# Kernel optimization log

Measured on AMD Instinct MI355X. Metric: run time of the kernel, lower is better.

## Reference

```python
import jax, jax.numpy as jnp
import numpy as np

VOCAB, E, H, L, B, T, S, V = 32000, 512, 1024, 2, 64, 64, 128, 1024
LSTM_IN = 2 * E  # input_feed=True -> cat(embed, prev_output)


def setup_inputs() -> dict:
    key = jax.random.key(0)
    ks = jax.random.split(key, 12)
    s = lambda *d: 1.0 / np.sqrt(d[-1])
    return {
        "tgt_batch": jax.random.randint(ks[0], (T, B), 0, VOCAB),
        "h_encoder": jax.random.normal(ks[1], (B, S, V), jnp.float32),
        "emb": jax.random.normal(ks[2], (VOCAB, E), jnp.float32) * 0.02,
        "output_init": jnp.zeros((B, E), jnp.float32),
        "hidden_init": jnp.zeros((L, B, H), jnp.float32),
        "W_ih": jax.random.uniform(ks[3], (L, 4 * H, LSTM_IN), jnp.float32, -s(H), s(H)),
        "W_hh": jax.random.uniform(ks[4], (L, 4 * H, H), jnp.float32, -s(H), s(H)),
        "b_ih": jax.random.uniform(ks[5], (L, 4 * H), jnp.float32, -s(H), s(H)),
        "b_hh": jax.random.uniform(ks[6], (L, 4 * H), jnp.float32, -s(H), s(H)),
        "W1": jax.random.uniform(ks[7], (V, H), jnp.float32, -s(H), s(H)),   # query_size->values_size
        "b1": jnp.zeros((V,), jnp.float32),
        "W2": jax.random.uniform(ks[8], (E, H + V), jnp.float32, -s(H + V), s(H + V)),
        "b2": jnp.zeros((E,), jnp.float32),
    }


def reference(tgt_batch, h_encoder, emb, output_init, hidden_init,
              W_ih, W_hh, b_ih, b_hh, W1, b1, W2, b2):
    x_seq = emb[tgt_batch]  # [T, B, E]

    def lstm_cell(x, h, c):  # x:[B,2E], h/c:[L,B,H]
        hs, cs, inp = [], [], x
        for l in range(L):
            gates = inp @ W_ih[l].T + b_ih[l] + h[l] @ W_hh[l].T + b_hh[l]
            i, f, g, o = jnp.split(gates, 4, axis=-1)  # torch gate order i,f,g,o
            c_new = jax.nn.sigmoid(f) * c[l] + jax.nn.sigmoid(i) * jnp.tanh(g)
            h_new = jax.nn.sigmoid(o) * jnp.tanh(c_new)
            hs.append(h_new); cs.append(c_new); inp = h_new
        return jnp.stack(hs), jnp.stack(cs), inp

    def global_attn(query):  # query:[B,H]
        q = query @ W1.T + b1                              # [B,V]
        scores = jnp.einsum('bv,bsv->bs', q, h_encoder)    # [B,S]
        a = jax.nn.softmax(scores, axis=-1)
        attended = jnp.einsum('bs,bsv->bv', a, h_encoder)  # [B,V]
        return jnp.tanh(jnp.concatenate([attended, query], axis=-1) @ W2.T + b2)

    def step(carry, x):
        h, c, out = carry
        inp = jnp.concatenate([x, out], axis=-1)  # input feed
        h, c, top = lstm_cell(inp, h, c)
        o = global_attn(top)  # dropout is identity in eval mode
        return (h, c, o), o

    c0 = jnp.zeros_like(hidden_init)
    _, outs = jax.lax.scan(step, (hidden_init, c0, output_init), x_seq)
    return jnp.transpose(outs, (1, 0, 2))  # [B, T, E]
```

## Files before the change

### kernel.cpp

```cpp
#include <hip/hip_runtime.h>

typedef _Float16 f16;
typedef f16 f16x8 __attribute__((ext_vector_type(8)));
typedef f16 f16x2 __attribute__((ext_vector_type(2)));
typedef float f32x4 __attribute__((ext_vector_type(4)));
typedef unsigned long long u64;

#define MFMA16(a, b, c) __builtin_amdgcn_mfma_f32_16x16x32_f16(a, b, c, 0, 0, 0)
#define ROT 16

__device__ inline float fsig(float x) { return 1.f / (1.f + __expf(-x)); }
__device__ inline float ftanh(float x) {
    x = fminf(15.f, fmaxf(-15.f, x));
    float e = __expf(2.f * x);
    return (e - 1.f) / (e + 1.f);
}

__device__ __forceinline__ void bstore8(void* p, u64 v) {
    __hip_atomic_store((u64*)p, v, __ATOMIC_RELAXED, __HIP_MEMORY_SCOPE_AGENT);
}
__device__ __forceinline__ void bstore4(float* p, float v) {
    __hip_atomic_store(p, v, __ATOMIC_RELAXED, __HIP_MEMORY_SCOPE_AGENT);
}
__device__ __forceinline__ float bload_f32(const float* p) {
    return __hip_atomic_load((float*)p, __ATOMIC_RELAXED, __HIP_MEMORY_SCOPE_AGENT);
}
__device__ __forceinline__ void fstore_u32(unsigned* p, unsigned v) {
    __hip_atomic_store(p, v, __ATOMIC_RELAXED, __HIP_MEMORY_SCOPE_AGENT);
}
__device__ __forceinline__ unsigned fload_u32(unsigned* p) {
    return __hip_atomic_load(p, __ATOMIC_RELAXED, __HIP_MEMORY_SCOPE_AGENT);
}

__global__ __launch_bounds__(256) void k_convert(
    const float* __restrict__ Wih, const float* __restrict__ Whh,
    const float* __restrict__ W1, const float* __restrict__ W2,
    const float* __restrict__ bih, const float* __restrict__ bhh,
    const int* __restrict__ tgt, const float* __restrict__ emb,
    const float* __restrict__ henc,
    f16* __restrict__ wcat, f16* __restrict__ w1c, f16* __restrict__ w2a,
    f16* __restrict__ w2b, float* __restrict__ bsum, f16* __restrict__ Xall,
    f16* __restrict__ h16)
{
    const long NW = 16777216, NT = 1048576, NA = 524288, NB = 524288,
               NS = 8192, NX = 2097152, NH = 8388608;
    const long TOT = NW + NT + NA + NB + NS + NX + NH;
    for (long i = (long)blockIdx.x * 256 + threadIdx.x; i < TOT;
         i += (long)gridDim.x * 256) {
        if (i < NW) {
            long l = i >> 23;
            long r = i & 8388607;
            int j = (int)(r >> 11), k = (int)(r & 2047);
            float val = (k < 1024) ? Wih[(l * 4096 + j) * 1024 + k]
                                   : Whh[(l * 4096 + j) * 1024 + (k - 1024)];
            wcat[i] = (f16)val;
        } else if (i < NW + NT) {
            long r = i - NW;
            int h = (int)(r >> 10), v = (int)(r & 1023);
            w1c[r] = (f16)W1[(long)v * 1024 + h];
        } else if (i < NW + NT + NA) {
            long r = i - NW - NT;
            int e = (int)(r >> 10), v = (int)(r & 1023);
            w2a[r] = (f16)W2[(long)e * 2048 + v];
        } else if (i < NW + NT + NA + NB) {
            long r = i - NW - NT - NA;
            int e = (int)(r >> 10), k = (int)(r & 1023);
            w2b[r] = (f16)W2[(long)e * 2048 + 1024 + k];
        } else if (i < NW + NT + NA + NB + NS) {
            long r = i - NW - NT - NA - NB;
            bsum[r] = bih[r] + bhh[r];
        } else if (i < NW + NT + NA + NB + NS + NX) {
            long r = i - NW - NT - NA - NB - NS;
            int t = (int)(r >> 15), mm = (int)((r >> 9) & 63), k = (int)(r & 511);
            Xall[r] = (f16)emb[(long)tgt[t * 64 + mm] * 512 + k];
        } else {
            long r = i - NW - NT - NA - NB - NS - NX;
            h16[r] = (f16)henc[r];
        }
    }
}

__global__ __launch_bounds__(256) void k_init(
    const float* __restrict__ oinit, const float* __restrict__ hinit,
    f16* __restrict__ O0, f16* __restrict__ H00, f16* __restrict__ H10,
    float* __restrict__ c01, unsigned* __restrict__ sync)
{
    int idx = blockIdx.x * 256 + threadIdx.x;
    if (idx < 32768) {
        O0[idx] = (f16)oinit[idx];
    } else if (idx < 98304) {
        H00[idx - 32768] = (f16)hinit[idx - 32768];
    } else if (idx < 163840) {
        H10[idx - 98304] = (f16)hinit[65536 + (idx - 98304)];
    } else if (idx < 294912) {
        c01[idx - 163840] = 0.f;
    } else if (idx < 297984) {
        sync[idx - 294912] = 0u;
    }
}

__global__ __launch_bounds__(256) void k_sb(
    const float* __restrict__ b1, const float* __restrict__ henc,
    float* __restrict__ sb)
{
    int bs = blockIdx.x * 256 + threadIdx.x;
    const float* hr = henc + (long)bs * 1024;
    float a = 0.f;
    for (int k = 0; k < 1024; k += 4) {
        float4 h4 = *(const float4*)(hr + k);
        float4 b4 = *(const float4*)(b1 + k);
        a += h4.x * b4.x + h4.y * b4.y + h4.z * b4.z + h4.w * b4.w;
    }
    sb[bs] = a;
}

__global__ __launch_bounds__(256) void k_gemm(
    const f16* __restrict__ A, const f16* __restrict__ Bm,
    f16* __restrict__ C, int N)
{
    int nb = N >> 7;
    int bm = blockIdx.x / nb, bn = blockIdx.x % nb;
    int tid = threadIdx.x, w = tid >> 6, lane = tid & 63;
    int quad = lane >> 4, nn = lane & 15;
    const f16* ap = A + (long)(bm * 64 + w * 16 + nn) * 1024 + quad * 8;
    const f16* bp = Bm + (long)(bn * 128 + nn) * 1024 + quad * 8;
    f32x4 acc[8] = {};
    for (int kk = 0; kk < 1024; kk += 32) {
        f16x8 av = *(const f16x8*)(ap + kk);
        #pragma unroll
        for (int t2 = 0; t2 < 8; ++t2) {
            f16x8 bv = *(const f16x8*)(bp + (long)t2 * 16 * 1024 + kk);
            acc[t2] = MFMA16(av, bv, acc[t2]);
        }
    }
    #pragma unroll
    for (int t2 = 0; t2 < 8; ++t2)
        #pragma unroll
        for (int r = 0; r < 4; ++r) {
            int m = bm * 64 + w * 16 + quad * 4 + r;
            int col = bn * 128 + t2 * 16 + nn;
            C[(long)m * N + col] = (f16)acc[t2][r];
        }
}

__device__ __forceinline__ void gsync(unsigned* sync, unsigned e) {
    asm volatile("s_waitcnt vmcnt(0) lgkmcnt(0)" ::: "memory");
    __syncthreads();
    unsigned* arr = sync;
    unsigned* rel = sync + 256;
    if (threadIdx.x == 0)
        fstore_u32(arr + blockIdx.x, e);
    if (blockIdx.x == 0) {
        if (threadIdx.x < 64) {
            int lane = threadIdx.x;
            for (;;) {
                unsigned v0 = fload_u32(arr + lane);
                unsigned v1 = fload_u32(arr + 64 + lane);
                unsigned v2 = fload_u32(arr + 128 + lane);
                unsigned v3 = fload_u32(arr + 192 + lane);
                if (__all((int)(v0 >= e && v1 >= e && v2 >= e && v3 >= e)))
                    break;
                __builtin_amdgcn_s_sleep(1);
            }
            if (lane < 8) fstore_u32(rel + lane * 32, e);
        }
    } else if (threadIdx.x == 0) {
        unsigned* r = rel + (blockIdx.x & 7) * 32;
        while (fload_u32(r) < e)
            __builtin_amdgcn_s_sleep(2);
    }
    __syncthreads();
    asm volatile("" ::: "memory");
}

__device__ __forceinline__ void lstm_core(
    const f16* base, int rst, const f16x8* wreg,
    const float* __restrict__ bs_, float* __restrict__ c_,
    f16* __restrict__ dest, float* lds, int b, int tid)
{
    int w = tid >> 6, lane = tid & 63, quad = lane >> 4, n = lane & 15;
    const f16* ap = base + (long)n * rst + quad * 8;
    f32x4 acc0 = {}, acc1 = {}, acc2 = {}, acc3 = {};
    #pragma unroll
    for (int kk = 0; kk < 8; ++kk) {
        f16x8 bv = wreg[kk];
        f16x8 a0 = *(const f16x8*)(ap + kk * 32);
        f16x8 a1 = *(const f16x8*)(ap + (long)16 * rst + kk * 32);
        f16x8 a2 = *(const f16x8*)(ap + (long)32 * rst + kk * 32);
        f16x8 a3 = *(const f16x8*)(ap + (long)48 * rst + kk * 32);
        acc0 = MFMA16(a0, bv, acc0);
        acc1 = MFMA16(a1, bv, acc1);
        acc2 = MFMA16(a2, bv, acc2);
        acc3 = MFMA16(a3, bv, acc3);
    }
    #pragma unroll
    for (int r = 0; r < 4; ++r) {
        int mb = quad * 4 + r;
        lds[(w * 64 + mb) * 17 + n]      = acc0[r];
        lds[(w * 64 + 16 + mb) * 17 + n] = acc1[r];
        lds[(w * 64 + 32 + mb) * 17 + n] = acc2[r];
        lds[(w * 64 + 48 + mb) * 17 + n] = acc3[r];
    }
    __syncthreads();
    if (tid < 256) {
        int m = tid >> 2, uu = tid & 3;
        float s0 = 0.f, s1 = 0.f, s2 = 0.f, s3 = 0.f;
        #pragma unroll
        for (int ww = 0; ww < 8; ++ww) {
            const float* p = lds + (ww * 64 + m) * 17 + uu * 4;
            s0 += p[0]; s1 += p[1]; s2 += p[2]; s3 += p[3];
        }
        int ug = b * 4 + uu;
        float iv = fsig(s0 + bs_[ug]);
        float fv = fsig(s1 + bs_[1024 + ug]);
        float gv = ftanh(s2 + bs_[2048 + ug]);
        float ov = fsig(s3 + bs_[3072 + ug]);
        float cold = c_[m * 1024 + ug];
        float cn = fv * cold + iv * gv;
        float hn = ov * ftanh(cn);
        c_[m * 1024 + ug] = cn;
        lds[8704 + m * 4 + uu] = hn;
    }
    __syncthreads();
    if (tid < 64) {
        union { f16 h[4]; u64 u; } pk;
        #pragma unroll
        for (int uu = 0; uu < 4; ++uu) pk.h[uu] = (f16)lds[8704 + tid * 4 + uu];
        bstore8(dest + (long)tid * 1024 + b * 4, pk.u);
    }
}

__device__ __forceinline__ void z1_core(
    const f16* __restrict__ H1n, const f16x8* wz, const float* __restrict__ b2,
    float* __restrict__ Z1f, int bb, int khalf, float* lds, int tid)
{
    int w = tid >> 6, lane = tid & 63, quad = lane >> 4, n = lane & 15;
    const f16* ap = H1n + (long)n * 1024 + khalf * 512 + w * 64 + quad * 8;
    f32x4 acc0 = {}, acc1 = {}, acc2 = {}, acc3 = {};
    #pragma unroll
    for (int kk = 0; kk < 2; ++kk) {
        f16x8 bv = wz[kk];
        f16x8 a0 = *(const f16x8*)(ap + kk * 32);
        f16x8 a1 = *(const f16x8*)(ap + 16384 + kk * 32);
        f16x8 a2 = *(const f16x8*)(ap + 32768 + kk * 32);
        f16x8 a3 = *(const f16x8*)(ap + 49152 + kk * 32);
        acc0 = MFMA16(a0, bv, acc0);
        acc1 = MFMA16(a1, bv, acc1);
        acc2 = MFMA16(a2, bv, acc2);
        acc3 = MFMA16(a3, bv, acc3);
    }
    #pragma unroll
    for (int r = 0; r < 4; ++r) {
        int mb = quad * 4 + r;
        lds[(w * 64 + mb) * 17 + n]      = acc0[r];
        lds[(w * 64 + 16 + mb) * 17 + n] = acc1[r];
        lds[(w * 64 + 32 + mb) * 17 + n] = acc2[r];
        lds[(w * 64 + 48 + mb) * 17 + n] = acc3[r];
    }
    __syncthreads();
    int m = tid >> 3, n0 = (tid & 7) * 2;
    float s0 = 0.f, s1 = 0.f;
    #pragma unroll
    for (int ww = 0; ww < 8; ++ww) {
        const float* p = lds + (ww * 64 + m) * 17 + n0;
        s0 += p[0]; s1 += p[1];
    }
    int e = bb * 16 + n0;
    if (khalf == 0) { s0 += b2[e]; s1 += b2[e + 1]; }
    union { float f[2]; u64 u; } pk;
    pk.f[0] = s0; pk.f[1] = s1;
    bstore8(Z1f + khalf * 32768 + (long)m * 512 + e, pk.u);
}

__global__ __launch_bounds__(512, 2) void k_persist(
    const f16* __restrict__ wcat, const float* __restrict__ bsum,
    float* __restrict__ c01, const f16* __restrict__ Xall,
    f16* __restrict__ Orot, f16* __restrict__ H0rot, f16* __restrict__ H1rot,
    const f16* __restrict__ P16, const f16* __restrict__ Q216,
    const f16* __restrict__ w2b, const float* __restrict__ sb,
    const float* __restrict__ b2, float* __restrict__ out,
    float* __restrict__ Z1f, float* __restrict__ Z2p,
    float* __restrict__ Sc, unsigned* __restrict__ sync)
{
    extern __shared__ float smem[];
    float* scr = smem;
    f16* Pl  = (f16*)(smem + 8960);
    f16* Q2l = Pl + 32768;

    int b = blockIdx.x, tid = threadIdx.x;
    int m = b >> 2, sq = b & 3;
    int wv = tid >> 6, lane = tid & 63, quad = lane >> 4, nn = lane & 15;
    unsigned* cnt = sync + 1024;

    f16x8 w0[8], w1[8];
    {
        int j0 = (nn & 3) * 1024 + b * 4 + (nn >> 2);
        const f16* wp = wcat + (long)j0 * 2048 + wv * 256 + quad * 8;
        #pragma unroll
        for (int kk = 0; kk < 8; ++kk) {
            w0[kk] = *(const f16x8*)(wp + kk * 32);
            w1[kk] = *(const f16x8*)(wp + 8388608 + kk * 32);
        }
    }
    f16x8 wz[2];
    if (b >= 64 && b < 128) {
        int zb = b - 64, bb = zb & 31, kh = zb >> 5;
        int j = bb * 16 + nn;
        const f16* zp = w2b + (long)j * 1024 + kh * 512 + wv * 64 + quad * 8;
        #pragma unroll
        for (int kk = 0; kk < 2; ++kk) wz[kk] = *(const f16x8*)(zp + kk * 32);
    }
    {
        const uint4* gp = (const uint4*)(P16 + ((long)(m * 128 + sq * 32)) * 1024);
        #pragma unroll
        for (int i = 0; i < 8; ++i) ((uint4*)Pl)[i * 512 + tid] = gp[i * 512 + tid];
        const uint4* gq = (const uint4*)(Q216 + ((long)(m * 128 + sq * 32)) * 512);
        #pragma unroll
        for (int i = 0; i < 4; ++i) ((uint4*)Q2l)[i * 512 + tid] = gq[i * 512 + tid];
    }
    __syncthreads();

    unsigned epoch = 0;
    for (int t = 0; t < 64; ++t) {
        int rs0 = t & (ROT - 1), rs1 = (t + 1) & (ROT - 1);
        const f16* Xc = Xall + (long)t * 32768;
        const f16* Oc = Orot + (long)rs0 * 32768;
        const f16* H0c = H0rot + (long)rs0 * 65536;
        f16* H0n = H0rot + (long)rs1 * 65536;
        const f16* H1c = H1rot + (long)rs0 * 65536;
        f16* H1n = H1rot + (long)rs1 * 65536;

        {
            const f16* base; int rst;
            if (wv < 2)      { base = Xc + wv * 256;        rst = 512; }
            else if (wv < 4) { base = Oc + (wv - 2) * 256;  rst = 512; }
            else             { base = H0c + (wv - 4) * 256; rst = 1024; }
            lstm_core(base, rst, w0, bsum, c01, H0n, scr, b, tid);
        }
        gsync(sync, ++epoch);

        {
            const f16* base = (wv < 4) ? (H0n + wv * 256) : (H1c + (wv - 4) * 256);
            lstm_core(base, 1024, w1, bsum + 4096, c01 + 65536, H1n, scr, b, tid);
        }
        gsync(sync, ++epoch);

        {
            f16* h1l = (f16*)scr;
            if (tid < 128)
                ((uint4*)h1l)[tid] = *(const uint4*)(H1n + (long)m * 1024 + tid * 8);
            __syncthreads();
            int sl = tid >> 4, kc = tid & 15;
            const f16* prow = Pl + sl * 1024;
            float a0 = 0.f;
            #pragma unroll
            for (int i = 0; i < 8; ++i) {
                int ch = (i * 16 + kc) * 8;
                f16x8 pv = *(const f16x8*)(prow + ch);
                f16x8 hv = *(const f16x8*)(h1l + ch);
                #pragma unroll
                for (int p2 = 0; p2 < 4; ++p2) {
                    f16x2 pa = { pv[p2 * 2], pv[p2 * 2 + 1] };
                    f16x2 ha = { hv[p2 * 2], hv[p2 * 2 + 1] };
                    a0 = __builtin_amdgcn_fdot2(pa, ha, a0, false);
                }
            }
            #pragma unroll
            for (int off = 8; off; off >>= 1) a0 += __shfl_xor(a0, off, 16);
            if (kc == 0)
                bstore4(Sc + m * 128 + sq * 32 + sl, a0 + sb[m * 128 + sq * 32 + sl]);
            __syncthreads();
            if (b >= 64 && b < 128)
                z1_core(H1n, wz, b2, Z1f, (b - 64) & 31, (b - 64) >> 5, scr, tid);
        }
        gsync(sync, ++epoch);

        {
            if (tid < 128) scr[tid] = bload_f32(Sc + m * 128 + tid);
            __syncthreads();
            if (tid < 64) {
                float v = fmaxf(scr[tid], scr[64 + tid]);
                #pragma unroll
                for (int off = 32; off; off >>= 1) v = fmaxf(v, __shfl_down(v, off));
                if (tid == 0) scr[128] = v;
            }
            __syncthreads();
            if (tid < 128) scr[tid] = __expf(scr[tid] - scr[128]);
            __syncthreads();
            if (tid < 64) {
                float v = scr[tid] + scr[64 + tid];
                #pragma unroll
                for (int off = 32; off; off >>= 1) v += __shfl_down(v, off);
                if (tid == 0) scr[129] = 1.f / v;
            }
            __syncthreads();
            float inv = scr[129];
            float zp = 0.f;
            #pragma unroll 8
            for (int jy = 0; jy < 32; ++jy)
                zp += scr[sq * 32 + jy] * (float)Q2l[jy * 512 + tid];
            bstore4(Z2p + ((m * 4 + sq) << 9) + tid, zp * inv);
            asm volatile("s_waitcnt vmcnt(0)" ::: "memory");
            __syncthreads();
            if (tid == 0) {
                unsigned old = __hip_atomic_fetch_add(cnt + m * 32, 1u,
                        __ATOMIC_RELAXED, __HIP_MEMORY_SCOPE_AGENT);
                scr[130] = (old == (unsigned)(4 * t + 3)) ? 1.f : 0.f;
            }
            __syncthreads();
            if (scr[130] != 0.f) {
                float z = bload_f32(Z1f + (m << 9) + tid)
                        + bload_f32(Z1f + 32768 + (m << 9) + tid);
                #pragma unroll
                for (int q = 0; q < 4; ++q)
                    z += bload_f32(Z2p + ((m * 4 + q) << 9) + tid);
                float o = ftanh(z);
                out[((long)m * 64 + t) * 512 + tid] = o;
                f16* ob = (f16*)(scr + 192);
                ob[tid] = (f16)o;
                __syncthreads();
                if (tid < 128) {
                    union { f16 h[4]; u64 u; } pk;
                    #pragma unroll
                    for (int i = 0; i < 4; ++i) pk.h[i] = ob[tid * 4 + i];
                    bstore8(Orot + (long)rs1 * 32768 + m * 512 + tid * 4, pk.u);
                }
            }
        }
        gsync(sync, ++epoch);
    }
}

extern "C" void kernel_launch(void* const* d_in, const int* in_sizes, int n_in,
                              void* d_out, int out_size, void* d_ws, size_t ws_size,
                              hipStream_t stream)
{
    const int*   tgt   = (const int*)d_in[0];
    const float* henc  = (const float*)d_in[1];
    const float* emb   = (const float*)d_in[2];
    const float* oinit = (const float*)d_in[3];
    const float* hinit = (const float*)d_in[4];
    const float* Wih   = (const float*)d_in[5];
    const float* Whh   = (const float*)d_in[6];
    const float* bih   = (const float*)d_in[7];
    const float* bhh   = (const float*)d_in[8];
    const float* W1    = (const float*)d_in[9];
    const float* b1    = (const float*)d_in[10];
    const float* W2    = (const float*)d_in[11];
    const float* b2    = (const float*)d_in[12];
    float* out = (float*)d_out;

    char* ws = (char*)d_ws;
    f16*      wcat  = (f16*)(ws + 0);
    f16*      P16   = (f16*)(ws + 33554432);
    f16*      Q216  = (f16*)(ws + 50331648);
    f16*      h16   = (f16*)(ws + 58720256);
    f16*      w2b   = (f16*)(ws + 75497472);
    f16*      w1c   = (f16*)(ws + 76546048);
    f16*      w2a   = (f16*)(ws + 78643200);
    f16*      Xall  = (f16*)(ws + 79691776);
    f16*      H0rot = (f16*)(ws + 83886080);
    f16*      H1rot = (f16*)(ws + 85983232);
    f16*      Orot  = (f16*)(ws + 88080384);
    float*    c01   = (float*)(ws + 89128960);
    float*    Z1f   = (float*)(ws + 89653248);
    float*    Z2p   = (float*)(ws + 89915392);
    float*    Sc    = (float*)(ws + 90439680);
    float*    bsum  = (float*)(ws + 90472448);
    float*    sb    = (float*)(ws + 90505216);
    unsigned* sync  = (unsigned*)(ws + 90537984);

    hipLaunchKernelGGL(k_convert, dim3(4096), dim3(256), 0, stream,
                       Wih, Whh, W1, W2, bih, bhh, tgt, emb, henc,
                       wcat, w1c, w2a, w2b, bsum, Xall, h16);
    hipLaunchKernelGGL(k_init, dim3(1164), dim3(256), 0, stream,
                       oinit, hinit, Orot, H0rot, H1rot, c01, sync);
    hipLaunchKernelGGL(k_sb, dim3(32), dim3(256), 0, stream, b1, henc, sb);
    hipLaunchKernelGGL(k_gemm, dim3(128 * 8), dim3(256), 0, stream,
                       h16, w1c, P16, 1024);
    hipLaunchKernelGGL(k_gemm, dim3(128 * 4), dim3(256), 0, stream,
                       h16, w2a, Q216, 512);

    static const unsigned LDS_BYTES = 8960 * 4 + 32768 * 2 + 16384 * 2;
    hipFuncSetAttribute((const void*)k_persist,
                        hipFuncAttributeMaxDynamicSharedMemorySize, LDS_BYTES);
    void* args[] = { &wcat, &bsum, &c01, &Xall, &Orot, &H0rot, &H1rot, &P16,
                     &Q216, &w2b, &sb, &b2, &out, &Z1f, &Z2p, &Sc, &sync };
    hipLaunchCooperativeKernel((const void*)k_persist, dim3(256), dim3(512),
                               args, LDS_BYTES, stream);
}
```

Before: 2.380 ms.

## Replace two grid-wide barriers per step with per-producer flag synchronization

Removes the grid barriers after the attention-score/Z1 phase and after the output phase. In their place, per-block score flags, per-block Z1 flags and per-batch-row output flags are written with agent-scope stores and polled by only the consumers that need them. The LSTM layer-0 waves that read the previous output wait on that row's output flag through an LDS handoff, so later work can start without a full grid sync. This cuts barrier latency on the serial 64-step recurrence, but adds polling traffic and relies on relaxed atomics plus vmcnt waits being enough for memory ordering.

```diff
diff --git a/kernel.cpp b/kernel.cpp
--- a/kernel.cpp
+++ b/kernel.cpp
@@ -30,6 +30,29 @@
 }
 __device__ __forceinline__ unsigned fload_u32(unsigned* p) {
     return __hip_atomic_load(p, __ATOMIC_RELAXED, __HIP_MEMORY_SCOPE_AGENT);
+}
+__device__ __forceinline__ void lstore_u32(unsigned* p, unsigned v) {
+    __hip_atomic_store(p, v, __ATOMIC_RELAXED, __HIP_MEMORY_SCOPE_WORKGROUP);
+}
+__device__ __forceinline__ unsigned lload_u32(unsigned* p) {
+    return __hip_atomic_load(p, __ATOMIC_RELAXED, __HIP_MEMORY_SCOPE_WORKGROUP);
+}
+
+__device__ __forceinline__ void poll64x(unsigned* f, unsigned e, int lane) {
+    for (;;) {
+        unsigned v = fload_u32(f + lane);
+        if (__all((int)(v >= e))) break;
+        __builtin_amdgcn_s_sleep(2);
+    }
+    asm volatile("" ::: "memory");
+}
+__device__ __forceinline__ void poll4(unsigned* f, unsigned e, int lane) {
+    for (;;) {
+        unsigned v = fload_u32(f + (lane & 3));
+        if (__all((int)(v >= e))) break;
+        __builtin_amdgcn_s_sleep(1);
+    }
+    asm volatile("" ::: "memory");
 }
 
 __global__ __launch_bounds__(256) void k_convert(
@@ -284,13 +307,20 @@
 {
     extern __shared__ float smem[];
     float* scr = smem;
-    f16* Pl  = (f16*)(smem + 8960);
+    unsigned* ofd = (unsigned*)(smem + 8960);
+    f16* Pl  = (f16*)(smem + 8976);
     f16* Q2l = Pl + 32768;
 
     int b = blockIdx.x, tid = threadIdx.x;
     int m = b >> 2, sq = b & 3;
     int wv = tid >> 6, lane = tid & 63, quad = lane >> 4, nn = lane & 15;
-    unsigned* cnt = sync + 1024;
+
+    unsigned* sflag = sync + 512;
+    unsigned* zflag = sync + 768;
+    unsigned* oflag = sync + 832;
+    unsigned* cnt   = sync + 1024;
+
+    const bool zb = (b >= 64 && b < 128);
 
     f16x8 w0[8], w1[8];
     {
@@ -303,8 +333,8 @@
         }
     }
     f16x8 wz[2];
-    if (b >= 64 && b < 128) {
-        int zb = b - 64, bb = zb & 31, kh = zb >> 5;
+    if (zb) {
+        int zz = b - 64, bb = zz & 31, kh = zz >> 5;
         int j = bb * 16 + nn;
         const f16* zp = w2b + (long)j * 1024 + kh * 512 + wv * 64 + quad * 8;
         #pragma unroll
@@ -318,6 +348,7 @@
         #pragma unroll
         for (int i = 0; i < 4; ++i) ((uint4*)Q2l)[i * 512 + tid] = gq[i * 512 + tid];
     }
+    if (tid == 0) lstore_u32(ofd, 0u);
     __syncthreads();
 
     unsigned epoch = 0;
@@ -335,6 +366,14 @@
             if (wv < 2)      { base = Xc + wv * 256;        rst = 512; }
             else if (wv < 4) { base = Oc + (wv - 2) * 256;  rst = 512; }
             else             { base = H0c + (wv - 4) * 256; rst = 1024; }
+            if (wv == 2) {
+                poll64x(oflag, (unsigned)t, lane);
+                if (lane == 0) lstore_u32(ofd, (unsigned)(t + 1));
+            } else if (wv == 3) {
+                while (lload_u32(ofd) < (unsigned)(t + 1))
+                    __builtin_amdgcn_s_sleep(1);
+                asm volatile("" ::: "memory");
+            }
             lstm_core(base, rst, w0, bsum, c01, H0n, scr, b, tid);
         }
         gsync(sync, ++epoch);
@@ -369,13 +408,19 @@
             for (int off = 8; off; off >>= 1) a0 += __shfl_xor(a0, off, 16);
             if (kc == 0)
                 bstore4(Sc + m * 128 + sq * 32 + sl, a0 + sb[m * 128 + sq * 32 + sl]);
-            __syncthreads();
-            if (b >= 64 && b < 128)
+            asm volatile("s_waitcnt vmcnt(0)" ::: "memory");
+            __syncthreads();
+            if (tid == 0) fstore_u32(sflag + b, (unsigned)(t + 1));
+            if (zb) {
                 z1_core(H1n, wz, b2, Z1f, (b - 64) & 31, (b - 64) >> 5, scr, tid);
-        }
-        gsync(sync, ++epoch);
+                asm volatile("s_waitcnt vmcnt(0)" ::: "memory");
+                __syncthreads();
+                if (tid == 0) fstore_u32(zflag + (b - 64), (unsigned)(t + 1));
+            }
+        }
 
         {
+            if (wv < 2) poll4(sflag + m * 4, (unsigned)(t + 1), lane);
             if (tid < 128) scr[tid] = bload_f32(Sc + m * 128 + tid);
             __syncthreads();
             if (tid < 64) {
@@ -409,6 +454,8 @@
             }
             __syncthreads();
             if (scr[130] != 0.f) {
+                if (wv == 0) poll64x(zflag, (unsigned)(t + 1), lane);
+                __syncthreads();
                 float z = bload_f32(Z1f + (m << 9) + tid)
                         + bload_f32(Z1f + 32768 + (m << 9) + tid);
                 #pragma unroll
@@ -425,9 +472,11 @@
                     for (int i = 0; i < 4; ++i) pk.h[i] = ob[tid * 4 + i];
                     bstore8(Orot + (long)rs1 * 32768 + m * 512 + tid * 4, pk.u);
                 }
-            }
-        }
-        gsync(sync, ++epoch);
+                if (wv < 2) asm volatile("s_waitcnt vmcnt(0)" ::: "memory");
+                __syncthreads();
+                if (tid == 0) fstore_u32(oflag + m, (unsigned)(t + 1));
+            }
+        }
     }
 }
 
@@ -481,7 +530,7 @@
     hipLaunchKernelGGL(k_gemm, dim3(128 * 4), dim3(256), 0, stream,
                        h16, w2a, Q216, 512);
 
-    static const unsigned LDS_BYTES = 8960 * 4 + 32768 * 2 + 16384 * 2;
+    static const unsigned LDS_BYTES = 8976 * 4 + 32768 * 2 + 16384 * 2;
     hipFuncSetAttribute((const void*)k_persist,
                         hipFuncAttributeMaxDynamicSharedMemorySize, LDS_BYTES);
     void* args[] = { &wcat, &bsum, &c01, &Xall, &Orot, &H0rot, &H1rot, &P16,
```

Result: slower. 2.685 ms (+12.8%).

## Use split-softmax partials to drop a grid barrier per step and parallelize finalization

Applied to the files above, without the earlier changes.

Each block now computes a local softmax over its 32 encoder positions, keeping the local max and sum, and publishes the unnormalized attention partial. This removes the global score exchange and one grid-wide barrier per timestep. The W2 query projection is spread over 128 blocks in K-quarters and overlapped with the score phase. The final tanh output is computed by all four blocks per batch row, each handling 128 columns with a log-sum-exp merge, which replaces the atomic last-block-finishes scheme. In exchange there are more global reads in finalization and Z buffers reuse the h16 workspace region, which is assumed to be dead by then.

```diff
diff --git a/kernel.cpp b/kernel.cpp
--- a/kernel.cpp
+++ b/kernel.cpp
@@ -230,25 +230,21 @@
     }
 }
 
-__device__ __forceinline__ void z1_core(
-    const f16* __restrict__ H1n, const f16x8* wz, const float* __restrict__ b2,
-    float* __restrict__ Z1f, int bb, int khalf, float* lds, int tid)
+__device__ __forceinline__ void z1q(
+    const f16* __restrict__ H1n, f16x8 wz, const float* __restrict__ b2,
+    float* __restrict__ Z1f, int er, int kq, float* lds, int tid)
 {
     int w = tid >> 6, lane = tid & 63, quad = lane >> 4, n = lane & 15;
-    const f16* ap = H1n + (long)n * 1024 + khalf * 512 + w * 64 + quad * 8;
+    const f16* ap = H1n + (long)n * 1024 + kq * 256 + w * 32 + quad * 8;
     f32x4 acc0 = {}, acc1 = {}, acc2 = {}, acc3 = {};
-    #pragma unroll
-    for (int kk = 0; kk < 2; ++kk) {
-        f16x8 bv = wz[kk];
-        f16x8 a0 = *(const f16x8*)(ap + kk * 32);
-        f16x8 a1 = *(const f16x8*)(ap + 16384 + kk * 32);
-        f16x8 a2 = *(const f16x8*)(ap + 32768 + kk * 32);
-        f16x8 a3 = *(const f16x8*)(ap + 49152 + kk * 32);
-        acc0 = MFMA16(a0, bv, acc0);
-        acc1 = MFMA16(a1, bv, acc1);
-        acc2 = MFMA16(a2, bv, acc2);
-        acc3 = MFMA16(a3, bv, acc3);
-    }
+    f16x8 a0 = *(const f16x8*)(ap);
+    f16x8 a1 = *(const f16x8*)(ap + 16384);
+    f16x8 a2 = *(const f16x8*)(ap + 32768);
+    f16x8 a3 = *(const f16x8*)(ap + 49152);
+    acc0 = MFMA16(a0, wz, acc0);
+    acc1 = MFMA16(a1, wz, acc1);
+    acc2 = MFMA16(a2, wz, acc2);
+    acc3 = MFMA16(a3, wz, acc3);
     #pragma unroll
     for (int r = 0; r < 4; ++r) {
         int mb = quad * 4 + r;
@@ -258,18 +254,18 @@
         lds[(w * 64 + 48 + mb) * 17 + n] = acc3[r];
     }
     __syncthreads();
-    int m = tid >> 3, n0 = (tid & 7) * 2;
+    int mm = tid >> 3, n0 = (tid & 7) * 2;
     float s0 = 0.f, s1 = 0.f;
     #pragma unroll
     for (int ww = 0; ww < 8; ++ww) {
-        const float* p = lds + (ww * 64 + m) * 17 + n0;
+        const float* p = lds + (ww * 64 + mm) * 17 + n0;
         s0 += p[0]; s1 += p[1];
     }
-    int e = bb * 16 + n0;
-    if (khalf == 0) { s0 += b2[e]; s1 += b2[e + 1]; }
+    int e = er * 16 + n0;
+    if (kq == 0) { s0 += b2[e]; s1 += b2[e + 1]; }
     union { float f[2]; u64 u; } pk;
     pk.f[0] = s0; pk.f[1] = s1;
-    bstore8(Z1f + khalf * 32768 + (long)m * 512 + e, pk.u);
+    bstore8(Z1f + kq * 32768 + (long)mm * 512 + e, pk.u);
 }
 
 __global__ __launch_bounds__(512, 2) void k_persist(
@@ -280,17 +276,17 @@
     const f16* __restrict__ w2b, const float* __restrict__ sb,
     const float* __restrict__ b2, float* __restrict__ out,
     float* __restrict__ Z1f, float* __restrict__ Z2p,
-    float* __restrict__ Sc, unsigned* __restrict__ sync)
+    float* __restrict__ Z2s, unsigned* __restrict__ sync)
 {
     extern __shared__ float smem[];
     float* scr = smem;
-    f16* Pl  = (f16*)(smem + 8960);
+    f16* h1l = (f16*)(smem + 8960);
+    f16* Pl  = (f16*)(smem + 9472);
     f16* Q2l = Pl + 32768;
 
     int b = blockIdx.x, tid = threadIdx.x;
     int m = b >> 2, sq = b & 3;
     int wv = tid >> 6, lane = tid & 63, quad = lane >> 4, nn = lane & 15;
-    unsigned* cnt = sync + 1024;
 
     f16x8 w0[8], w1[8];
     {
@@ -302,13 +298,11 @@
             w1[kk] = *(const f16x8*)(wp + 8388608 + kk * 32);
         }
     }
-    f16x8 wz[2];
-    if (b >= 64 && b < 128) {
-        int zb = b - 64, bb = zb & 31, kh = zb >> 5;
-        int j = bb * 16 + nn;
-        const f16* zp = w2b + (long)j * 1024 + kh * 512 + wv * 64 + quad * 8;
-        #pragma unroll
-        for (int kk = 0; kk < 2; ++kk) wz[kk] = *(const f16x8*)(zp + kk * 32);
+    f16x8 wz = {};
+    if (b < 128) {
+        int er = b & 31, kq = b >> 5;
+        const f16* zp = w2b + (long)(er * 16 + nn) * 1024 + kq * 256 + wv * 32 + quad * 8;
+        wz = *(const f16x8*)zp;
     }
     {
         const uint4* gp = (const uint4*)(P16 + ((long)(m * 128 + sq * 32)) * 1024);
@@ -346,9 +340,10 @@
         gsync(sync, ++epoch);
 
         {
-            f16* h1l = (f16*)scr;
             if (tid < 128)
                 ((uint4*)h1l)[tid] = *(const uint4*)(H1n + (long)m * 1024 + tid * 8);
+            if (b < 128)
+                z1q(H1n, wz, b2, Z1f, b & 31, b >> 5, scr, tid);
             __syncthreads();
             int sl = tid >> 4, kc = tid & 15;
             const f16* prow = Pl + sl * 1024;
@@ -368,63 +363,64 @@
             #pragma unroll
             for (int off = 8; off; off >>= 1) a0 += __shfl_xor(a0, off, 16);
             if (kc == 0)
-                bstore4(Sc + m * 128 + sq * 32 + sl, a0 + sb[m * 128 + sq * 32 + sl]);
+                scr[8704 + sl] = a0 + sb[m * 128 + sq * 32 + sl];
             __syncthreads();
-            if (b >= 64 && b < 128)
-                z1_core(H1n, wz, b2, Z1f, (b - 64) & 31, (b - 64) >> 5, scr, tid);
-        }
-        gsync(sync, ++epoch);
-
-        {
-            if (tid < 128) scr[tid] = bload_f32(Sc + m * 128 + tid);
-            __syncthreads();
-            if (tid < 64) {
-                float v = fmaxf(scr[tid], scr[64 + tid]);
+            if (tid < 32) {
+                float v = scr[8704 + tid];
+                float mx = v;
                 #pragma unroll
-                for (int off = 32; off; off >>= 1) v = fmaxf(v, __shfl_down(v, off));
-                if (tid == 0) scr[128] = v;
+                for (int off = 16; off; off >>= 1) mx = fmaxf(mx, __shfl_xor(mx, off));
+                float ev = __expf(v - mx);
+                float sm = ev;
+                #pragma unroll
+                for (int off = 16; off; off >>= 1) sm += __shfl_xor(sm, off);
+                scr[8704 + tid] = ev;
+                if (tid == 0) {
+                    union { float f[2]; u64 u; } pk;
+                    pk.f[0] = mx; pk.f[1] = sm;
+                    bstore8(Z2s + ((m * 4 + sq) << 1), pk.u);
+                }
             }
             __syncthreads();
-            if (tid < 128) scr[tid] = __expf(scr[tid] - scr[128]);
-            __syncthreads();
-            if (tid < 64) {
-                float v = scr[tid] + scr[64 + tid];
-                #pragma unroll
-                for (int off = 32; off; off >>= 1) v += __shfl_down(v, off);
-                if (tid == 0) scr[129] = 1.f / v;
-            }
-            __syncthreads();
-            float inv = scr[129];
             float zp = 0.f;
             #pragma unroll 8
             for (int jy = 0; jy < 32; ++jy)
-                zp += scr[sq * 32 + jy] * (float)Q2l[jy * 512 + tid];
-            bstore4(Z2p + ((m * 4 + sq) << 9) + tid, zp * inv);
-            asm volatile("s_waitcnt vmcnt(0)" ::: "memory");
+                zp += scr[8704 + jy] * (float)Q2l[jy * 512 + tid];
+            bstore4(Z2p + ((m * 4 + sq) << 9) + tid, zp);
+        }
+        gsync(sync, ++epoch);
+
+        {
+            if (tid < 8) scr[8744 + tid] = bload_f32(Z2s + m * 8 + tid);
             __syncthreads();
-            if (tid == 0) {
-                unsigned old = __hip_atomic_fetch_add(cnt + m * 32, 1u,
-                        __ATOMIC_RELAXED, __HIP_MEMORY_SCOPE_AGENT);
-                scr[130] = (old == (unsigned)(4 * t + 3)) ? 1.f : 0.f;
+            if (tid < 128) {
+                float m0 = scr[8744], s0q = scr[8745], m1 = scr[8746], s1q = scr[8747],
+                      m2 = scr[8748], s2q = scr[8749], m3 = scr[8750], s3q = scr[8751];
+                float M = fmaxf(fmaxf(m0, m1), fmaxf(m2, m3));
+                float q0 = __expf(m0 - M), q1 = __expf(m1 - M),
+                      q2 = __expf(m2 - M), q3 = __expf(m3 - M);
+                float den = q0 * s0q + q1 * s1q + q2 * s2q + q3 * s3q;
+                int e = sq * 128 + tid;
+                float z = bload_f32(Z1f + (m << 9) + e)
+                        + bload_f32(Z1f + 32768 + (m << 9) + e)
+                        + bload_f32(Z1f + 65536 + (m << 9) + e)
+                        + bload_f32(Z1f + 98304 + (m << 9) + e);
+                float num = q0 * bload_f32(Z2p + ((m * 4 + 0) << 9) + e)
+                          + q1 * bload_f32(Z2p + ((m * 4 + 1) << 9) + e)
+                          + q2 * bload_f32(Z2p + ((m * 4 + 2) << 9) + e)
+                          + q3 * bload_f32(Z2p + ((m * 4 + 3) << 9) + e);
+                z += num / den;
+                float o = ftanh(z);
+                out[((long)m * 64 + t) * 512 + e] = o;
+                ((f16*)(scr + 8752))[tid] = (f16)o;
             }
             __syncthreads();
-            if (scr[130] != 0.f) {
-                float z = bload_f32(Z1f + (m << 9) + tid)
-                        + bload_f32(Z1f + 32768 + (m << 9) + tid);
+            if (tid < 32) {
+                f16* ob = (f16*)(scr + 8752);
+                union { f16 h[4]; u64 u; } pk;
                 #pragma unroll
-                for (int q = 0; q < 4; ++q)
-                    z += bload_f32(Z2p + ((m * 4 + q) << 9) + tid);
-                float o = ftanh(z);
-                out[((long)m * 64 + t) * 512 + tid] = o;
-                f16* ob = (f16*)(scr + 192);
-                ob[tid] = (f16)o;
-                __syncthreads();
-                if (tid < 128) {
-                    union { f16 h[4]; u64 u; } pk;
-                    #pragma unroll
-                    for (int i = 0; i < 4; ++i) pk.h[i] = ob[tid * 4 + i];
-                    bstore8(Orot + (long)rs1 * 32768 + m * 512 + tid * 4, pk.u);
-                }
+                for (int i = 0; i < 4; ++i) pk.h[i] = ob[tid * 4 + i];
+                bstore8(Orot + (long)rs1 * 32768 + m * 512 + sq * 128 + tid * 4, pk.u);
             }
         }
         gsync(sync, ++epoch);
@@ -463,9 +459,9 @@
     f16*      H1rot = (f16*)(ws + 85983232);
     f16*      Orot  = (f16*)(ws + 88080384);
     float*    c01   = (float*)(ws + 89128960);
-    float*    Z1f   = (float*)(ws + 89653248);
-    float*    Z2p   = (float*)(ws + 89915392);
-    float*    Sc    = (float*)(ws + 90439680);
+    float*    Z1f   = (float*)(ws + 58720256);
+    float*    Z2p   = (float*)(ws + 59244544);
+    float*    Z2s   = (float*)(ws + 90439680);
     float*    bsum  = (float*)(ws + 90472448);
     float*    sb    = (float*)(ws + 90505216);
     unsigned* sync  = (unsigned*)(ws + 90537984);
@@ -481,11 +477,11 @@
     hipLaunchKernelGGL(k_gemm, dim3(128 * 4), dim3(256), 0, stream,
                        h16, w2a, Q216, 512);
 
-    static const unsigned LDS_BYTES = 8960 * 4 + 32768 * 2 + 16384 * 2;
+    static const unsigned LDS_BYTES = 9472 * 4 + 32768 * 2 + 16384 * 2;
     hipFuncSetAttribute((const void*)k_persist,
                         hipFuncAttributeMaxDynamicSharedMemorySize, LDS_BYTES);
     void* args[] = { &wcat, &bsum, &c01, &Xall, &Orot, &H0rot, &H1rot, &P16,
-                     &Q216, &w2b, &sb, &b2, &out, &Z1f, &Z2p, &Sc, &sync };
+                     &Q216, &w2b, &sb, &b2, &out, &Z1f, &Z2p, &Z2s, &sync };
     hipLaunchCooperativeKernel((const void*)k_persist, dim3(256), dim3(512),
                                args, LDS_BYTES, stream);
 }
```

Measured after the change: 2.234 ms. 1.07x faster.
